# Performance work log

Measured on AMD Instinct MI355X. Metric: run time of the kernel, lower is better.

Reference implementation:

```python
import jax, jax.numpy as jnp
import numpy as np

POINT_NUM = 50000
MAX_DEGREE = 16
BATCH = 32


def setup_inputs() -> dict:
    key = jax.random.key(0)
    k1, k2, k3, k4 = jax.random.split(key, 4)
    predict_points = jax.random.normal(k1, (BATCH, POINT_NUM, 3), dtype=jnp.float32)
    gt_points = jax.random.normal(k2, (BATCH, POINT_NUM, 3), dtype=jnp.float32)
    # neighbour indices in [0, POINT_NUM]; index == POINT_NUM hits the zero-pad row
    neighbour = jax.random.randint(k3, (POINT_NUM, MAX_DEGREE), 0, POINT_NUM + 1, dtype=jnp.int64)
    degrees = jax.random.randint(k4, (POINT_NUM,), 0, MAX_DEGREE + 1, dtype=jnp.int32)
    return {
        "predict_points": predict_points,
        "gt_points": gt_points,
        "neighbour": neighbour,
        "degrees": degrees,
    }


def _laplacian(points, padded, neighbour, deg):
    # points: [B, N, 3]; padded: [B, N+1, 3]; neighbour: [N, D]; deg: [1, N, 1]
    nbr_sum = padded[:, neighbour, :].sum(axis=2)  # [B, N, D, 3] -> [B, N, 3]
    return points * deg - nbr_sum


def reference(predict_points, gt_points, neighbour, degrees):
    batch = predict_points.shape[0]
    zeros = jnp.zeros((batch, 1, 3), dtype=predict_points.dtype)
    padded_predict = jnp.concatenate([predict_points, zeros], axis=1)
    padded_gt = jnp.concatenate([gt_points, zeros], axis=1)
    deg = degrees.astype(predict_points.dtype)[None, :, None]  # [1, N, 1]
    gt_laplace = _laplacian(gt_points, padded_gt, neighbour, deg)
    predict_laplace = _laplacian(predict_points, padded_predict, neighbour, deg)
    diff = predict_laplace - gt_laplace  # [B, N, 3]
    loss = jnp.sqrt(jnp.sum(diff * diff, axis=2)).sum(axis=1).mean()
    return loss
```

## Files before the change

### kernel.cpp

```cpp
#include <hip/hip_runtime.h>
#include <hip/hip_fp16.h>
#include <math.h>

#define N_POINTS 50000
#define MAX_DEG 16
#define BATCH 32

struct alignas(8) H4 { __half2 a, b; };
#define DELTA_ELEMS ((size_t)(N_POINTS + 1) * BATCH)

__global__ __launch_bounds__(256) void delta_transpose_kernel(
    const float* __restrict__ predict,
    const float* __restrict__ gt,
    H4* __restrict__ delta)
{
    __shared__ __half s_h[32][100];

    const int t  = threadIdx.x;
    const int n0 = blockIdx.x * 32;

    {
        const int b = t >> 3;
        const int q = t & 7;
        const size_t base_f4 = ((size_t)b * (N_POINTS * 3) + (size_t)n0 * 3) >> 2;
        const float4* __restrict__ p4 = (const float4*)predict;
        const float4* __restrict__ g4 = (const float4*)gt;
        const int valid_f4 = ((N_POINTS - n0) * 3) >> 2;
        __half2* row2 = (__half2*)&s_h[b][0];
#pragma unroll
        for (int k = 0; k < 3; ++k) {
            const int j = k * 8 + q;
            float4 d = make_float4(0.f, 0.f, 0.f, 0.f);
            if (j < valid_f4) {
                const float4 p = p4[base_f4 + j];
                const float4 g = g4[base_f4 + j];
                d.x = p.x - g.x; d.y = p.y - g.y;
                d.z = p.z - g.z; d.w = p.w - g.w;
            }
            row2[j * 2 + 0] = __floats2half2_rn(d.x, d.y);
            row2[j * 2 + 1] = __floats2half2_rn(d.z, d.w);
        }
    }
    __syncthreads();

    {
        const int b = t & 31;
#pragma unroll
        for (int i = 0; i < 4; ++i) {
            const int nl = i * 8 + (t >> 5);
            const int n  = n0 + nl;
            if (n <= N_POINTS) {
                const __half h0 = s_h[b][nl * 3 + 0];
                const __half h1 = s_h[b][nl * 3 + 1];
                const __half h2 = s_h[b][nl * 3 + 2];
                H4 val;
                val.a = __halves2half2(h0, h1);
                val.b = __halves2half2(h2, __float2half(0.f));
                delta[(size_t)n * BATCH + b] = val;
            }
        }
    }
}

__global__ __launch_bounds__(256) void laplace_gather_kernel(
    const H4* __restrict__ delta,
    const int*  __restrict__ neighbour,
    const int*  __restrict__ degrees,
    float* __restrict__ partial)
{
    __shared__ int   s_nbr[8 * MAX_DEG];
    __shared__ float s_deg[8];
    __shared__ float s_part[4];

    const int t = threadIdx.x;
    const int n_base = blockIdx.x * 8;

    if (t < 8 * MAX_DEG)
        s_nbr[t] = neighbour[(size_t)n_base * MAX_DEG + t];
    if (t < 8)
        s_deg[t] = (float)degrees[n_base + t];
    __syncthreads();

    const int b  = t & 31;
    const int yn = t >> 5;
    const int n  = n_base + yn;

    const H4 c = delta[(size_t)n * BATCH + b];
    H4 v[MAX_DEG];
#pragma unroll
    for (int d = 0; d < MAX_DEG; ++d) {
        const int idx = s_nbr[yn * MAX_DEG + d];
        v[d] = delta[(size_t)idx * BATCH + b];
    }

    float sx = 0.f, sy = 0.f, sz = 0.f;
#pragma unroll
    for (int d = 0; d < MAX_DEG; ++d) {
        const float2 xy = __half22float2(v[d].a);
        sx += xy.x;
        sy += xy.y;
        sz += __low2float(v[d].b);
    }

    const float deg = s_deg[yn];
    const float2 cxy = __half22float2(c.a);
    const float  cz  = __low2float(c.b);
    const float ax = fmaf(cxy.x, deg, -sx);
    const float ay = fmaf(cxy.y, deg, -sy);
    const float az = fmaf(cz,    deg, -sz);

    float dist = sqrtf(ax * ax + ay * ay + az * az);

#pragma unroll
    for (int o = 32; o > 0; o >>= 1)
        dist += __shfl_down(dist, o, 64);

    if ((t & 63) == 0) s_part[t >> 6] = dist;
    __syncthreads();

    if (t == 0)
        partial[blockIdx.x] = s_part[0] + s_part[1] + s_part[2] + s_part[3];
}

__global__ __launch_bounds__(256) void final_reduce_kernel(
    const float* __restrict__ partial, float* __restrict__ out, int nparts)
{
    __shared__ float s_part[4];
    const int t = threadIdx.x;

    float acc = 0.f;
#pragma unroll 4
    for (int i = t; i < nparts; i += 256)
        acc += partial[i];

#pragma unroll
    for (int o = 32; o > 0; o >>= 1)
        acc += __shfl_down(acc, o, 64);

    if ((t & 63) == 0) s_part[t >> 6] = acc;
    __syncthreads();

    if (t == 0)
        out[0] = (s_part[0] + s_part[1] + s_part[2] + s_part[3]) * (1.0f / BATCH);
}

extern "C" void kernel_launch(void* const* d_in, const int* in_sizes, int n_in,
                              void* d_out, int out_size, void* d_ws, size_t ws_size,
                              hipStream_t stream)
{
    const float* predict   = (const float*)d_in[0];
    const float* gt        = (const float*)d_in[1];
    const int*   neighbour = (const int*)d_in[2];
    const int*   degrees   = (const int*)d_in[3];
    float* out = (float*)d_out;

    H4*    delta   = (H4*)d_ws;
    float* partial = (float*)(delta + DELTA_ELEMS);

    const int grid1 = (N_POINTS + 1 + 31) / 32;
    delta_transpose_kernel<<<grid1, 256, 0, stream>>>(predict, gt, delta);

    const int grid2 = N_POINTS / 8;
    laplace_gather_kernel<<<grid2, 256, 0, stream>>>(delta, neighbour, degrees, partial);

    final_reduce_kernel<<<1, 256, 0, stream>>>(partial, out, grid2);
}
```

Measured before the change: 112.5 us.

## Split delta buffer into per-batch-group slabs for cache-local neighbour gathers

The fp16 delta buffer is now stored as four slabs, each holding 8 batch entries per point, instead of one interleaved array of 32 batch entries. Each gather block handles 32 points for a single batch group, so every gathered row is 64 bytes and the working set each block touches is a quarter of the full buffer. This aims to improve L2 and MALL hit rates on the random neighbour gathers. In exchange, each neighbour index is loaded four times across groups and each gathered row is a smaller, less efficient memory access.

After: 111.0 us. No clear change (-1.3%).

```diff
diff --git a/kernel.cpp b/kernel.cpp
--- a/kernel.cpp
+++ b/kernel.cpp
@@ -5,9 +5,12 @@
 #define N_POINTS 50000
 #define MAX_DEG 16
 #define BATCH 32
+#define NGROUP 4
+#define GROUP_B 8
+#define SLAB ((size_t)(N_POINTS + 1))
 
 struct alignas(8) H4 { __half2 a, b; };
-#define DELTA_ELEMS ((size_t)(N_POINTS + 1) * BATCH)
+#define DELTA_ELEMS ((size_t)NGROUP * SLAB * GROUP_B)
 
 __global__ __launch_bounds__(256) void delta_transpose_kernel(
     const float* __restrict__ predict,
@@ -44,19 +47,18 @@
     __syncthreads();
 
     {
-        const int b = t & 31;
+        const int b  = t & 31;
+        const int g  = b >> 3;
+        const int bl = b & 7;
 #pragma unroll
         for (int i = 0; i < 4; ++i) {
             const int nl = i * 8 + (t >> 5);
             const int n  = n0 + nl;
             if (n <= N_POINTS) {
-                const __half h0 = s_h[b][nl * 3 + 0];
-                const __half h1 = s_h[b][nl * 3 + 1];
-                const __half h2 = s_h[b][nl * 3 + 2];
                 H4 val;
-                val.a = __halves2half2(h0, h1);
-                val.b = __halves2half2(h2, __float2half(0.f));
-                delta[(size_t)n * BATCH + b] = val;
+                val.a = __halves2half2(s_h[b][nl * 3 + 0], s_h[b][nl * 3 + 1]);
+                val.b = __halves2half2(s_h[b][nl * 3 + 2], __ushort_as_half(0));
+                delta[((size_t)g * SLAB + n) * GROUP_B + bl] = val;
             }
         }
     }
@@ -68,29 +70,40 @@
     const int*  __restrict__ degrees,
     float* __restrict__ partial)
 {
-    __shared__ int   s_nbr[8 * MAX_DEG];
-    __shared__ float s_deg[8];
+    __shared__ int   s_nbr[32 * 17];
+    __shared__ float s_deg[32];
     __shared__ float s_part[4];
 
-    const int t = threadIdx.x;
-    const int n_base = blockIdx.x * 8;
+    const int t    = threadIdx.x;
+    const int g    = blockIdx.x & 3;
+    const int nb   = (blockIdx.x >> 2) * 32;
 
-    if (t < 8 * MAX_DEG)
-        s_nbr[t] = neighbour[(size_t)n_base * MAX_DEG + t];
-    if (t < 8)
-        s_deg[t] = (float)degrees[n_base + t];
+#pragma unroll
+    for (int r = 0; r < 2; ++r) {
+        const int i  = t + r * 256;
+        const int pt = i >> 4, d = i & 15;
+        const int n  = nb + pt;
+        s_nbr[pt * 17 + d] = (n < N_POINTS) ? neighbour[(size_t)n * MAX_DEG + d]
+                                            : N_POINTS;
+    }
+    if (t < 32) {
+        const int n = nb + t;
+        s_deg[t] = (n < N_POINTS) ? (float)degrees[n] : 0.f;
+    }
     __syncthreads();
 
-    const int b  = t & 31;
-    const int yn = t >> 5;
-    const int n  = n_base + yn;
+    const int pt = t >> 3;
+    const int bl = t & 7;
+    const int n  = nb + pt;
+    const int nn = (n < N_POINTS) ? n : N_POINTS;
+    const H4* __restrict__ slab = delta + (size_t)g * SLAB * GROUP_B;
 
-    const H4 c = delta[(size_t)n * BATCH + b];
+    const H4 c = slab[(size_t)nn * GROUP_B + bl];
     H4 v[MAX_DEG];
 #pragma unroll
     for (int d = 0; d < MAX_DEG; ++d) {
-        const int idx = s_nbr[yn * MAX_DEG + d];
-        v[d] = delta[(size_t)idx * BATCH + b];
+        const int idx = s_nbr[pt * 17 + d];
+        v[d] = slab[(size_t)idx * GROUP_B + bl];
     }
 
     float sx = 0.f, sy = 0.f, sz = 0.f;
@@ -102,14 +115,13 @@
         sz += __low2float(v[d].b);
     }
 
-    const float deg = s_deg[yn];
+    const float deg = s_deg[pt];
     const float2 cxy = __half22float2(c.a);
-    const float  cz  = __low2float(c.b);
     const float ax = fmaf(cxy.x, deg, -sx);
     const float ay = fmaf(cxy.y, deg, -sy);
-    const float az = fmaf(cz,    deg, -sz);
+    const float az = fmaf(__low2float(c.b), deg, -sz);
 
-    float dist = sqrtf(ax * ax + ay * ay + az * az);
+    float dist = (n < N_POINTS) ? sqrtf(ax * ax + ay * ay + az * az) : 0.f;
 
 #pragma unroll
     for (int o = 32; o > 0; o >>= 1)
@@ -157,10 +169,10 @@
     H4*    delta   = (H4*)d_ws;
     float* partial = (float*)(delta + DELTA_ELEMS);
 
-    const int grid1 = (N_POINTS + 1 + 31) / 32;
-    delta_transpose_kernel<<<grid1, 256, 0, stream>>>(predict, gt, delta);
+    const int tiles = (N_POINTS + 1 + 31) / 32;
+    delta_transpose_kernel<<<tiles, 256, 0, stream>>>(predict, gt, delta);
 
-    const int grid2 = N_POINTS / 8;
+    const int grid2 = tiles * NGROUP;
     laplace_gather_kernel<<<grid2, 256, 0, stream>>>(delta, neighbour, degrees, partial);
 
     final_reduce_kernel<<<1, 256, 0, stream>>>(partial, out, grid2);
```
